# Kernel tuning notes

Measured on AMD Instinct MI355X. Metric: run time of the kernel, lower is better.

Reference implementation:

```python
import jax, jax.numpy as jnp
import numpy as np

NUM_LAYERS = 4
INPUT_SIZE = 1024
RNN_SIZE = 1024
BATCH = 128


def setup_inputs() -> dict:
    key = jax.random.key(0)
    ks = jax.random.split(key, 7)
    H4 = 4 * RNN_SIZE
    return {
        "x": jax.random.normal(ks[0], (BATCH, INPUT_SIZE), dtype=jnp.float32),
        "h0": jax.random.normal(ks[1], (NUM_LAYERS, BATCH, RNN_SIZE), dtype=jnp.float32),
        "c0": jax.random.normal(ks[2], (NUM_LAYERS, BATCH, RNN_SIZE), dtype=jnp.float32),
        "W_ih": jax.random.normal(ks[3], (NUM_LAYERS, H4, INPUT_SIZE), dtype=jnp.float32) * 0.02,
        "W_hh": jax.random.normal(ks[4], (NUM_LAYERS, H4, RNN_SIZE), dtype=jnp.float32) * 0.02,
        "b_ih": jax.random.normal(ks[5], (NUM_LAYERS, H4), dtype=jnp.float32) * 0.02,
        "b_hh": jax.random.normal(ks[6], (NUM_LAYERS, H4), dtype=jnp.float32) * 0.02,
    }


def _lstm_cell(x, h, c, w_ih, w_hh, bi, bh):
    # gates: [B, 4H], PyTorch LSTMCell order (i, f, g, o)
    gates = x @ w_ih.T + bi + h @ w_hh.T + bh
    i, f, g, o = jnp.split(gates, 4, axis=-1)
    i = jax.nn.sigmoid(i)
    f = jax.nn.sigmoid(f)
    g = jnp.tanh(g)
    o = jax.nn.sigmoid(o)
    c1 = f * c + i * g
    h1 = o * jnp.tanh(c1)
    return h1, c1


def reference(x, h0, c0, W_ih, W_hh, b_ih, b_hh):
    # Stacked single-timestep LSTM with input feeding (dropout=0.0 -> identity).
    inp = x
    h1s, c1s = [], []
    for i in range(NUM_LAYERS):
        h1, c1 = _lstm_cell(inp, h0[i], c0[i], W_ih[i], W_hh[i], b_ih[i], b_hh[i])
        inp = h1  # dropout(p=0) is identity between layers
        h1s.append(h1)
        c1s.append(c1)
    return inp, jnp.stack(h1s), jnp.stack(c1s)
```

## Files before the change

kernel.cpp:

```cpp
#include <hip/hip_runtime.h>

#define NLAYER 4
#define B_ 128
#define D_ 1024
#define H4_ 4096
#define K_ 2048
#define OUTSEC 131072
#define CH_PER 8
#define GP_STRIDE 524288

typedef float f32x4 __attribute__((ext_vector_type(4)));
typedef _Float16 h8 __attribute__((ext_vector_type(8)));
typedef _Float16 h4 __attribute__((ext_vector_type(4)));

struct ALF { h8 v[4]; };
struct W4  { f32x4 a, b, c, d; };

__device__ __forceinline__ void stage16(const void* gsrc, char* lds_uniform, int lane) {
#if __has_builtin(__builtin_amdgcn_global_load_lds)
  __builtin_amdgcn_global_load_lds((const __attribute__((address_space(1))) void*)gsrc,
                                   (__attribute__((address_space(3))) void*)lds_uniform,
                                   16, 0, 0);
#else
  *(h8*)(lds_uniform + lane * 16) = *(const h8*)gsrc;
#endif
}

__global__ __launch_bounds__(256)
void prep_kernel(const float* __restrict__ x, const float* __restrict__ h0,
                 const float* __restrict__ bih, const float* __restrict__ bhh,
                 _Float16* __restrict__ Ah, _Float16* __restrict__ Al,
                 float* __restrict__ b4)
{
  if (blockIdx.x >= 640) {
    int idx = (blockIdx.x - 640) * 256 + threadIdx.x;
    int l = idx >> 10, u = idx & 1023;
    f32x4 r;
#pragma unroll
    for (int q = 0; q < 4; ++q)
      r[q] = bih[l * H4_ + q * D_ + u] + bhh[l * H4_ + q * D_ + u];
    *(f32x4*)(b4 + (size_t)idx * 4) = r;
    return;
  }
  int i = (blockIdx.x * 256 + threadIdx.x) * 4;
  const float* src;
  int dst;
  if (i < 131072) {
    int b = i >> 10, k = i & 1023;
    src = x + i;
    dst = b * K_ + k;
  } else {
    int j = i - 131072;
    int l = j >> 17, r = j & 131071;
    int b = r >> 10, k = r & 1023;
    src = h0 + j;
    dst = l * (B_ * K_) + b * K_ + D_ + k;
  }
  f32x4 v = *(const f32x4*)src;
  h4 hi, lo;
#pragma unroll
  for (int j2 = 0; j2 < 4; ++j2) {
    _Float16 h = (_Float16)v[j2];
    hi[j2] = h;
    lo[j2] = (_Float16)((v[j2] - (float)h) * 4096.0f);
  }
  *(h4*)(Ah + dst) = hi;
  *(h4*)(Al + dst) = lo;
}

__global__ __launch_bounds__(256, 4)
void gemm_part(const float* __restrict__ Wih, const float* __restrict__ Whh,
               const _Float16* __restrict__ Ah, const _Float16* __restrict__ Al,
               float* __restrict__ gp)
{
  __shared__ __align__(16) char smem[32768];
  const int tid  = threadIdx.x;
  const int lane = tid & 63;
  const int wid  = tid >> 6;
  const int bidx = blockIdx.x;
  const int s    = bidx & 3;
  const int nt   = bidx >> 2;
  const int u0   = nt * 4;
  const int k0   = s * 512;

  const int n16 = lane & 15;
  const int kq  = lane >> 4;
  const int wr  = ((n16 & 3) << 10) + u0 + (n16 >> 2);
  const float* wbase = (s < 2) ? (Wih + k0) : (Whh + (k0 - 1024));
  const float* wp = wbase + (size_t)wr * D_ + kq * 8;

  const int R0   = wid * 32 + (lane >> 3);
  const int cswz = ((lane & 7) ^ (lane >> 3)) * 8;
  const _Float16* ahg = Ah + (size_t)R0 * K_ + k0 + cswz;

  const int arow = wid * 32 + n16;
  const int aswz = (lane & 7) << 4;
  const _Float16* alg = Al + (size_t)arow * K_ + k0 + kq * 8;

  f32x4 acc_h[2] = {{0.f,0.f,0.f,0.f},{0.f,0.f,0.f,0.f}};
  f32x4 acc_s[2] = {{0.f,0.f,0.f,0.f},{0.f,0.f,0.f,0.f}};

  auto loadW = [&](int t) -> W4 {
    const float* p = wp + t * 64;
    W4 r;
    r.a = *(const f32x4*)(p);
    r.b = *(const f32x4*)(p + 4);
    r.c = *(const f32x4*)(p + 32);
    r.d = *(const f32x4*)(p + 36);
    return r;
  };
  auto stageA = [&](int t, int buf) {
    const _Float16* g = ahg + t * 64;
    char* lb = smem + buf * 16384 + wid * 4096;
    stage16(g,            lb,        lane);
    stage16(g +  8 * K_,  lb + 1024, lane);
    stage16(g + 16 * K_,  lb + 2048, lane);
    stage16(g + 24 * K_,  lb + 3072, lane);
  };
  auto loadAL = [&](int t) -> ALF {
    ALF r;
#pragma unroll
    for (int m = 0; m < 2; ++m)
#pragma unroll
      for (int ks = 0; ks < 2; ++ks)
        r.v[m * 2 + ks] = *(const h8*)(alg + (size_t)m * 16 * K_ + t * 64 + ks * 32);
    return r;
  };

  W4  wreg = loadW(0);
  ALF alf[2];
  alf[0] = loadAL(0);
  stageA(0, 0);
  __syncthreads();

#pragma unroll
  for (int t = 0; t < CH_PER; ++t) {
    h8 whi[2], wlo[2];
    {
      const f32x4* wv = &wreg.a;
#pragma unroll
      for (int ks = 0; ks < 2; ++ks)
#pragma unroll
        for (int j = 0; j < 8; ++j) {
          float f = wv[ks * 2 + (j >> 2)][j & 3];
          _Float16 h = (_Float16)f;
          whi[ks][j] = h;
          wlo[ks][j] = (_Float16)((f - (float)h) * 4096.0f);
        }
    }
    if (t + 1 < CH_PER) {
      stageA(t + 1, (t + 1) & 1);
      alf[(t + 1) & 1] = loadAL(t + 1);
      wreg = loadW(t + 1);
    }
    {
      const char* ab = smem + (t & 1) * 16384;
      h8 a[2][2];
#pragma unroll
      for (int ks = 0; ks < 2; ++ks)
#pragma unroll
        for (int m = 0; m < 2; ++m)
          a[m][ks] = *(const h8*)(ab + (arow + m * 16) * 128 + ((ks * 64 + kq * 16) ^ aswz));
#pragma unroll
      for (int m = 0; m < 2; ++m)
#pragma unroll
        for (int ks = 0; ks < 2; ++ks) {
          acc_h[m] = __builtin_amdgcn_mfma_f32_16x16x32_f16(a[m][ks],             whi[ks], acc_h[m], 0, 0, 0);
          acc_s[m] = __builtin_amdgcn_mfma_f32_16x16x32_f16(alf[t & 1].v[m*2+ks], whi[ks], acc_s[m], 0, 0, 0);
          acc_s[m] = __builtin_amdgcn_mfma_f32_16x16x32_f16(a[m][ks],             wlo[ks], acc_s[m], 0, 0, 0);
        }
    }
    __syncthreads();
  }

  const float INV = 1.0f / 4096.0f;
  float* gout = gp + (size_t)s * GP_STRIDE + (size_t)(nt * 16 + n16);
#pragma unroll
  for (int m = 0; m < 2; ++m)
#pragma unroll
    for (int j = 0; j < 4; ++j) {
      int row = wid * 32 + m * 16 + kq * 4 + j;
      gout[(size_t)row * H4_] = acc_h[m][j] + acc_s[m][j] * INV;
    }
}

__global__ __launch_bounds__(256)
void cell_kernel(const float* __restrict__ gp, const float* __restrict__ b4,
                 const float* __restrict__ c0, float* __restrict__ out,
                 _Float16* __restrict__ AhN, _Float16* __restrict__ AlN, int layer)
{
  int i = blockIdx.x * 256 + threadIdx.x;
  int row = i >> 10, u = i & 1023;
  int c4 = ((u >> 2) << 4) + ((u & 3) << 2);
  const float* g0 = gp + (size_t)row * H4_ + c4;
  f32x4 g = *(const f32x4*)(g0);
  g += *(const f32x4*)(g0 + GP_STRIDE);
  g += *(const f32x4*)(g0 + 2 * (size_t)GP_STRIDE);
  g += *(const f32x4*)(g0 + 3 * (size_t)GP_STRIDE);
  f32x4 bb = *(const f32x4*)(b4 + (size_t)u * 4);
  float gi = g[0] + bb[0];
  float gf = g[1] + bb[1];
  float gg = g[2] + bb[2];
  float go = g[3] + bb[3];
  float iv = 1.0f / (1.0f + __expf(-gi));
  float fv = 1.0f / (1.0f + __expf(-gf));
  float gv = tanhf(gg);
  float ov = 1.0f / (1.0f + __expf(-go));
  float c0v = c0[i];
  float c1  = fv * c0v + iv * gv;
  float h1v = ov * tanhf(c1);
  out[(5 + layer) * OUTSEC + i] = c1;
  out[(1 + layer) * OUTSEC + i] = h1v;
  if (layer == 3) {
    out[i] = h1v;
  } else {
    _Float16 hh = (_Float16)h1v;
    AhN[(size_t)row * K_ + u] = hh;
    AlN[(size_t)row * K_ + u] = (_Float16)((h1v - (float)hh) * 4096.0f);
  }
}

extern "C" void kernel_launch(void* const* d_in, const int* in_sizes, int n_in,
                              void* d_out, int out_size, void* d_ws, size_t ws_size,
                              hipStream_t stream)
{
  const float* x   = (const float*)d_in[0];
  const float* h0  = (const float*)d_in[1];
  const float* c0  = (const float*)d_in[2];
  const float* Wih = (const float*)d_in[3];
  const float* Whh = (const float*)d_in[4];
  const float* bih = (const float*)d_in[5];
  const float* bhh = (const float*)d_in[6];
  float* out = (float*)d_out;

  _Float16* Ah = (_Float16*)d_ws;
  _Float16* Al = Ah + 4 * B_ * K_;
  float* gp = (float*)((char*)d_ws + 4u * 1024 * 1024);
  float* b4 = (float*)((char*)d_ws + 12u * 1024 * 1024);

  prep_kernel<<<656, 256, 0, stream>>>(x, h0, bih, bhh, Ah, Al, b4);
  for (int l = 0; l < NLAYER; ++l) {
    gemm_part<<<1024, 256, 0, stream>>>(
        Wih + (size_t)l * H4_ * D_, Whh + (size_t)l * H4_ * D_,
        Ah + (size_t)l * B_ * K_, Al + (size_t)l * B_ * K_, gp);
    cell_kernel<<<512, 256, 0, stream>>>(
        gp, b4 + (size_t)l * 4096, c0 + (size_t)l * OUTSEC, out,
        (l < 3) ? Ah + (size_t)(l + 1) * B_ * K_ : (_Float16*)nullptr,
        (l < 3) ? Al + (size_t)(l + 1) * B_ * K_ : (_Float16*)nullptr, l);
  }
}
```

Measured before the change: 302.0 us.

## Store activations in MFMA-fragment order and load directly from global

The fp16 hi/lo activation buffers are now written by the prep and cell kernels in a pre-tiled layout that matches the MFMA A-operand fragment order. This lets the GEMM kernel read each fragment with one coalesced 16-byte global load per lane. LDS staging, the double buffer, the swizzle and the barriers are removed. Software prefetch of weights and activations across iterations is also dropped, so latency hiding now depends on the compiler and on occupancy. The cell kernel's scattered fp16 writes into the tiled layout may coalesce less well.

```diff
diff --git a/kernel.cpp b/kernel.cpp
--- a/kernel.cpp
+++ b/kernel.cpp
@@ -6,24 +6,15 @@
 #define H4_ 4096
 #define K_ 2048
 #define OUTSEC 131072
-#define CH_PER 8
 #define GP_STRIDE 524288
+#define AL_STRIDE 262144
 
 typedef float f32x4 __attribute__((ext_vector_type(4)));
 typedef _Float16 h8 __attribute__((ext_vector_type(8)));
 typedef _Float16 h4 __attribute__((ext_vector_type(4)));
 
-struct ALF { h8 v[4]; };
-struct W4  { f32x4 a, b, c, d; };
-
-__device__ __forceinline__ void stage16(const void* gsrc, char* lds_uniform, int lane) {
-#if __has_builtin(__builtin_amdgcn_global_load_lds)
-  __builtin_amdgcn_global_load_lds((const __attribute__((address_space(1))) void*)gsrc,
-                                   (__attribute__((address_space(3))) void*)lds_uniform,
-                                   16, 0, 0);
-#else
-  *(h8*)(lds_uniform + lane * 16) = *(const h8*)gsrc;
-#endif
+__device__ __forceinline__ int amoff(int row, int k) {
+  return ((k >> 5) * 8 + (row >> 4)) * 512 + (((k >> 3) & 3) * 16 + (row & 15)) * 8 + (k & 7);
 }
 
 __global__ __launch_bounds__(256)
@@ -44,17 +35,16 @@
   }
   int i = (blockIdx.x * 256 + threadIdx.x) * 4;
   const float* src;
-  int dst;
+  int l, row, k;
   if (i < 131072) {
-    int b = i >> 10, k = i & 1023;
+    l = 0; row = i >> 10; k = i & 1023;
     src = x + i;
-    dst = b * K_ + k;
   } else {
     int j = i - 131072;
-    int l = j >> 17, r = j & 131071;
-    int b = r >> 10, k = r & 1023;
+    l = j >> 17;
+    int r = j & 131071;
+    row = r >> 10; k = (r & 1023) + D_;
     src = h0 + j;
-    dst = l * (B_ * K_) + b * K_ + D_ + k;
   }
   f32x4 v = *(const f32x4*)src;
   h4 hi, lo;
@@ -64,8 +54,9 @@
     hi[j2] = h;
     lo[j2] = (_Float16)((v[j2] - (float)h) * 4096.0f);
   }
-  *(h4*)(Ah + dst) = hi;
-  *(h4*)(Al + dst) = lo;
+  int off = l * AL_STRIDE + amoff(row, k);
+  *(h4*)(Ah + off) = hi;
+  *(h4*)(Al + off) = lo;
 }
 
 __global__ __launch_bounds__(256, 4)
@@ -73,13 +64,11 @@
                const _Float16* __restrict__ Ah, const _Float16* __restrict__ Al,
                float* __restrict__ gp)
 {
-  __shared__ __align__(16) char smem[32768];
   const int tid  = threadIdx.x;
   const int lane = tid & 63;
   const int wid  = tid >> 6;
-  const int bidx = blockIdx.x;
-  const int s    = bidx & 3;
-  const int nt   = bidx >> 2;
+  const int s    = blockIdx.x & 3;
+  const int nt   = blockIdx.x >> 2;
   const int u0   = nt * 4;
   const int k0   = s * 512;
 
@@ -89,92 +78,48 @@
   const float* wbase = (s < 2) ? (Wih + k0) : (Whh + (k0 - 1024));
   const float* wp = wbase + (size_t)wr * D_ + kq * 8;
 
-  const int R0   = wid * 32 + (lane >> 3);
-  const int cswz = ((lane & 7) ^ (lane >> 3)) * 8;
-  const _Float16* ahg = Ah + (size_t)R0 * K_ + k0 + cswz;
-
-  const int arow = wid * 32 + n16;
-  const int aswz = (lane & 7) << 4;
-  const _Float16* alg = Al + (size_t)arow * K_ + k0 + kq * 8;
+  const char* afh0 = (const char*)Ah + (size_t)(s * 16) * 8192 + (wid * 2) * 1024 + lane * 16;
+  const char* afl0 = (const char*)Al + (size_t)(s * 16) * 8192 + (wid * 2) * 1024 + lane * 16;
 
   f32x4 acc_h[2] = {{0.f,0.f,0.f,0.f},{0.f,0.f,0.f,0.f}};
   f32x4 acc_s[2] = {{0.f,0.f,0.f,0.f},{0.f,0.f,0.f,0.f}};
 
-  auto loadW = [&](int t) -> W4 {
+  for (int t = 0; t < 8; ++t) {
     const float* p = wp + t * 64;
-    W4 r;
-    r.a = *(const f32x4*)(p);
-    r.b = *(const f32x4*)(p + 4);
-    r.c = *(const f32x4*)(p + 32);
-    r.d = *(const f32x4*)(p + 36);
-    return r;
-  };
-  auto stageA = [&](int t, int buf) {
-    const _Float16* g = ahg + t * 64;
-    char* lb = smem + buf * 16384 + wid * 4096;
-    stage16(g,            lb,        lane);
-    stage16(g +  8 * K_,  lb + 1024, lane);
-    stage16(g + 16 * K_,  lb + 2048, lane);
-    stage16(g + 24 * K_,  lb + 3072, lane);
-  };
-  auto loadAL = [&](int t) -> ALF {
-    ALF r;
+    f32x4 w0 = *(const f32x4*)(p);
+    f32x4 w1 = *(const f32x4*)(p + 4);
+    f32x4 w2 = *(const f32x4*)(p + 32);
+    f32x4 w3 = *(const f32x4*)(p + 36);
+    h8 ah[2][2], al[2][2];
 #pragma unroll
-    for (int m = 0; m < 2; ++m)
+    for (int ks = 0; ks < 2; ++ks)
 #pragma unroll
-      for (int ks = 0; ks < 2; ++ks)
-        r.v[m * 2 + ks] = *(const h8*)(alg + (size_t)m * 16 * K_ + t * 64 + ks * 32);
-    return r;
-  };
-
-  W4  wreg = loadW(0);
-  ALF alf[2];
-  alf[0] = loadAL(0);
-  stageA(0, 0);
-  __syncthreads();
-
+      for (int m = 0; m < 2; ++m) {
+        int bo = (t * 2 + ks) * 8192 + m * 1024;
+        ah[m][ks] = *(const h8*)(afh0 + bo);
+        al[m][ks] = *(const h8*)(afl0 + bo);
+      }
 #pragma unroll
-  for (int t = 0; t < CH_PER; ++t) {
-    h8 whi[2], wlo[2];
-    {
-      const f32x4* wv = &wreg.a;
+    for (int ks = 0; ks < 2; ++ks) {
+      h8 whi, wlo;
 #pragma unroll
-      for (int ks = 0; ks < 2; ++ks)
+      for (int j = 0; j < 8; ++j) {
+        float f = (j < 4) ? (ks ? w2[j] : w0[j]) : (ks ? w3[j - 4] : w1[j - 4]);
+        _Float16 h = (_Float16)f;
+        whi[j] = h;
+        wlo[j] = (_Float16)((f - (float)h) * 4096.0f);
+      }
 #pragma unroll
-        for (int j = 0; j < 8; ++j) {
-          float f = wv[ks * 2 + (j >> 2)][j & 3];
-          _Float16 h = (_Float16)f;
-          whi[ks][j] = h;
-          wlo[ks][j] = (_Float16)((f - (float)h) * 4096.0f);
-        }
+      for (int m = 0; m < 2; ++m) {
+        acc_h[m] = __builtin_amdgcn_mfma_f32_16x16x32_f16(ah[m][ks], whi, acc_h[m], 0, 0, 0);
+        acc_s[m] = __builtin_amdgcn_mfma_f32_16x16x32_f16(al[m][ks], whi, acc_s[m], 0, 0, 0);
+        acc_s[m] = __builtin_amdgcn_mfma_f32_16x16x32_f16(ah[m][ks], wlo, acc_s[m], 0, 0, 0);
+      }
     }
-    if (t + 1 < CH_PER) {
-      stageA(t + 1, (t + 1) & 1);
-      alf[(t + 1) & 1] = loadAL(t + 1);
-      wreg = loadW(t + 1);
-    }
-    {
-      const char* ab = smem + (t & 1) * 16384;
-      h8 a[2][2];
-#pragma unroll
-      for (int ks = 0; ks < 2; ++ks)
-#pragma unroll
-        for (int m = 0; m < 2; ++m)
-          a[m][ks] = *(const h8*)(ab + (arow + m * 16) * 128 + ((ks * 64 + kq * 16) ^ aswz));
-#pragma unroll
-      for (int m = 0; m < 2; ++m)
-#pragma unroll
-        for (int ks = 0; ks < 2; ++ks) {
-          acc_h[m] = __builtin_amdgcn_mfma_f32_16x16x32_f16(a[m][ks],             whi[ks], acc_h[m], 0, 0, 0);
-          acc_s[m] = __builtin_amdgcn_mfma_f32_16x16x32_f16(alf[t & 1].v[m*2+ks], whi[ks], acc_s[m], 0, 0, 0);
-          acc_s[m] = __builtin_amdgcn_mfma_f32_16x16x32_f16(a[m][ks],             wlo[ks], acc_s[m], 0, 0, 0);
-        }
-    }
-    __syncthreads();
   }
 
   const float INV = 1.0f / 4096.0f;
-  float* gout = gp + (size_t)s * GP_STRIDE + (size_t)(nt * 16 + n16);
+  float* gout = gp + (size_t)s * GP_STRIDE + nt * 16 + n16;
 #pragma unroll
   for (int m = 0; m < 2; ++m)
 #pragma unroll
@@ -215,8 +160,9 @@
     out[i] = h1v;
   } else {
     _Float16 hh = (_Float16)h1v;
-    AhN[(size_t)row * K_ + u] = hh;
-    AlN[(size_t)row * K_ + u] = (_Float16)((h1v - (float)hh) * 4096.0f);
+    int off = amoff(row, u);
+    AhN[off] = hh;
+    AlN[off] = (_Float16)((h1v - (float)hh) * 4096.0f);
   }
 }
 
@@ -234,18 +180,18 @@
   float* out = (float*)d_out;
 
   _Float16* Ah = (_Float16*)d_ws;
-  _Float16* Al = Ah + 4 * B_ * K_;
-  float* gp = (float*)((char*)d_ws + 4u * 1024 * 1024);
-  float* b4 = (float*)((char*)d_ws + 12u * 1024 * 1024);
+  _Float16* Al = Ah + 4 * AL_STRIDE;
+  float* gp = (float*)((char*)d_ws + (4u << 20));
+  float* b4 = (float*)((char*)d_ws + (12u << 20));
 
   prep_kernel<<<656, 256, 0, stream>>>(x, h0, bih, bhh, Ah, Al, b4);
   for (int l = 0; l < NLAYER; ++l) {
     gemm_part<<<1024, 256, 0, stream>>>(
         Wih + (size_t)l * H4_ * D_, Whh + (size_t)l * H4_ * D_,
-        Ah + (size_t)l * B_ * K_, Al + (size_t)l * B_ * K_, gp);
+        Ah + (size_t)l * AL_STRIDE, Al + (size_t)l * AL_STRIDE, gp);
     cell_kernel<<<512, 256, 0, stream>>>(
         gp, b4 + (size_t)l * 4096, c0 + (size_t)l * OUTSEC, out,
-        (l < 3) ? Ah + (size_t)(l + 1) * B_ * K_ : (_Float16*)nullptr,
-        (l < 3) ? Al + (size_t)(l + 1) * B_ * K_ : (_Float16*)nullptr, l);
+        (l < 3) ? Ah + (size_t)(l + 1) * AL_STRIDE : (_Float16*)nullptr,
+        (l < 3) ? Al + (size_t)(l + 1) * AL_STRIDE : (_Float16*)nullptr, l);
   }
 }
```

Result: faster. 280.5 us (-7.1%).
